# Optimization experiments

Hardware: AMD Instinct MI355X
Metric: run time of the kernel (lower is better)

The kernel has to match this reference:

```python
import jax, jax.numpy as jnp
import numpy as np

B, T, D, H = 2, 2048, 1024, 16
DK = D // H


def setup_inputs() -> dict:
    key = jax.random.key(0)
    ks = jax.random.split(key, 12)
    q = jax.random.normal(ks[0], (B, T, D), jnp.float32)
    k = jax.random.normal(ks[1], (B, T, D), jnp.float32)
    v = jax.random.normal(ks[2], (B, T, D), jnp.float32)
    # padding mask [B,1,T]: 1 = valid, 0 = pad (nonzero per torch eq(0) semantics)
    lengths = jnp.array([T, (3 * T) // 4])
    mask = (jnp.arange(T)[None, None, :] < lengths[:, None, None]).astype(jnp.int32)
    s = 0.02
    Wq = jax.random.normal(ks[3], (D, D), jnp.float32) * s
    Wk = jax.random.normal(ks[4], (D, D), jnp.float32) * s
    Wv = jax.random.normal(ks[5], (D, D), jnp.float32) * s
    Wo = jax.random.normal(ks[6], (D, D), jnp.float32) * s
    bq = jnp.zeros((D,), jnp.float32)
    bk = jnp.zeros((D,), jnp.float32)
    bv = jnp.zeros((D,), jnp.float32)
    bo = jnp.zeros((D,), jnp.float32)
    return {"query": q, "key": k, "value": v, "mask": mask,
            "Wq": Wq, "bq": bq, "Wk": Wk, "bk": bk,
            "Wv": Wv, "bv": bv, "Wo": Wo, "bo": bo}


def reference(query, key, value, mask, Wq, bq, Wk, bk, Wv, bv, Wo, bo):
    # q,k,v projections -> [B, H, T, DK]
    def proj(x, W, b):
        return (x @ W.T + b).reshape(B, T, H, DK).transpose(0, 2, 1, 3)
    q = proj(query, Wq, bq)
    k = proj(key, Wk, bk)
    v = proj(value, Wv, bv)
    scores = jnp.einsum("bhqd,bhkd->bhqk", q, k) * (DK ** -0.5)  # [B,H,T,T]
    m = (mask == 0)[:, None, :, :]  # [B,1,1,T] broadcast over heads/queries
    scores = jnp.where(m, -jnp.inf, scores)
    attn = jax.nn.softmax(scores, axis=-1)
    attn = jnp.where(m, 0.0, attn)
    x = jnp.einsum("bhqk,bhkd->bhqd", attn, v)  # [B,H,T,DK]
    x = x.transpose(0, 2, 1, 3).reshape(B, T, D)
    return x @ Wo.T + bo
```

## Files before the change

### kernel.cpp

```cpp
#include <hip/hip_runtime.h>

typedef unsigned short u16;
typedef unsigned int u32;
typedef __bf16 bf16x8 __attribute__((ext_vector_type(8)));
typedef float floatx4 __attribute__((ext_vector_type(4)));

#define BB 2
#define TT 2048
#define DD 1024
#define HH 16
#define DKK 64
#define ACT (BB * TT * DD)
#define WTE (DD * DD)

__device__ inline u16 f2bf(float f) {
    union { float f; u32 u; } c; c.f = f;
    u32 r = (c.u + 0x7fffu + ((c.u >> 16) & 1u)) >> 16;
    return (u16)r;
}
__device__ inline u32 pack2bf(float a, float b) {
    return (u32)f2bf(a) | ((u32)f2bf(b) << 16);
}

typedef __attribute__((address_space(1))) const u32 gas_u32;
typedef __attribute__((address_space(3))) u32 las_u32;
__device__ __forceinline__ void gl2lds16(const u16* g, u16* l) {
    __builtin_amdgcn_global_load_lds((gas_u32*)g, (las_u32*)l, 16, 0, 0);
}

struct CvtArgs { const float* src[7]; u16* dst[7]; };
__global__ __launch_bounds__(256) void convert_bf16(CvtArgs a) {
    int bid = blockIdx.x, t, local;
    if (bid < 768) { t = bid >> 8; local = bid & 255; }
    else { int r = bid - 768; t = 3 + (r >> 6); local = r & 63; }
    const float* s = a.src[t];
    u16* d = a.dst[t];
    const int base = local * 16384;
    for (int i = 0; i < 8; i++) {
        const int idx = base + i * 2048 + threadIdx.x * 8;
        float4 x0 = *(const float4*)(s + idx);
        float4 x1 = *(const float4*)(s + idx + 4);
        uint4 p;
        p.x = pack2bf(x0.x, x0.y); p.y = pack2bf(x0.z, x0.w);
        p.z = pack2bf(x1.x, x1.y); p.w = pack2bf(x1.z, x1.w);
        *(uint4*)(d + idx) = p;
    }
}

__global__ __launch_bounds__(256) void qkv_gemm(
    const u16* __restrict__ Qc, const u16* __restrict__ Kc,
    const u16* __restrict__ Vc,
    const u16* __restrict__ Wqc, const u16* __restrict__ Wkc,
    const u16* __restrict__ Wvc,
    const float* __restrict__ bq, const float* __restrict__ bk,
    const float* __restrict__ bv,
    u16* __restrict__ ws)
{
    __shared__ __align__(16) u16 As[128 * 32];
    __shared__ __align__(16) u16 Bs[128 * 32];
    const int z = blockIdx.z;
    const u16* A = (z == 0) ? Qc : (z == 1) ? Kc : Vc;
    const u16* W = (z == 0) ? Wqc : (z == 1) ? Wkc : Wvc;
    const float* bias = (z == 0) ? bq : (z == 1) ? bk : bv;
    u16* out = ws + (size_t)z * ACT / 4;
    out = ws + (size_t)z * (size_t)BB * HH * TT * DKK;

    const int tid  = threadIdx.x;
    const int wave = tid >> 6, lane = tid & 63;
    const int quad = lane >> 4, l16 = lane & 15;
    const int wm = wave & 1, wn = wave >> 1;
    const int m0 = blockIdx.y * 128, n0 = blockIdx.x * 128;
    const int K = DD;

    const int lrow = lane >> 2, lcol = (lane & 3) * 8;
    const u16* Ag0 = A + (size_t)(m0 + wave * 16 + lrow) * K + lcol;
    const u16* Ag1 = A + (size_t)(m0 + 64 + wave * 16 + lrow) * K + lcol;
    const u16* Wg0 = W + (size_t)(n0 + wave * 16 + lrow) * K + lcol;
    const u16* Wg1 = W + (size_t)(n0 + 64 + wave * 16 + lrow) * K + lcol;
    u16* AsD0 = &As[(wave * 16) * 32];
    u16* AsD1 = &As[(64 + wave * 16) * 32];
    u16* BsD0 = &Bs[(wave * 16) * 32];
    u16* BsD1 = &Bs[(64 + wave * 16) * 32];

    floatx4 acc[4][4];
    for (int i = 0; i < 4; i++)
        for (int j = 0; j < 4; j++)
            acc[i][j] = floatx4{0.f, 0.f, 0.f, 0.f};

    for (int k0 = 0; k0 < K; k0 += 32) {
        __syncthreads();
        gl2lds16(Ag0 + k0, AsD0);
        gl2lds16(Ag1 + k0, AsD1);
        gl2lds16(Wg0 + k0, BsD0);
        gl2lds16(Wg1 + k0, BsD1);
        __syncthreads();

        bf16x8 af[4], bfr[4];
        for (int mi = 0; mi < 4; mi++)
            af[mi] = *(const bf16x8*)&As[(wm * 64 + mi * 16 + l16) * 32 + quad * 8];
        for (int ni = 0; ni < 4; ni++)
            bfr[ni] = *(const bf16x8*)&Bs[(wn * 64 + ni * 16 + l16) * 32 + quad * 8];
        for (int mi = 0; mi < 4; mi++)
            for (int ni = 0; ni < 4; ni++)
                acc[mi][ni] = __builtin_amdgcn_mfma_f32_16x16x32_bf16(
                    af[mi], bfr[ni], acc[mi][ni], 0, 0, 0);
    }

    for (int ni = 0; ni < 4; ni++) {
        const int n = n0 + wn * 64 + ni * 16 + l16;
        const float bv2 = bias[n];
        for (int mi = 0; mi < 4; mi++) {
            for (int vv = 0; vv < 4; vv++) {
                const int m = m0 + wm * 64 + mi * 16 + quad * 4 + vv;
                const float val = acc[mi][ni][vv] + bv2;
                const int b = m >> 11, t = m & 2047, h = n >> 6, dk = n & 63;
                if (z == 2)
                    out[(((size_t)(b * HH + h)) * DKK + dk) * TT + t] = f2bf(val);
                else
                    out[(((size_t)(b * HH + h)) * TT + t) * DKK + dk] = f2bf(val);
            }
        }
    }
}

__global__ __launch_bounds__(256) void out_gemm(
    const u16* __restrict__ Av, const u16* __restrict__ Wv,
    const float* __restrict__ bias, float* __restrict__ outv)
{
    __shared__ __align__(16) u16 As[128 * 32];
    __shared__ __align__(16) u16 Bs[128 * 32];
    const int tid  = threadIdx.x;
    const int wave = tid >> 6, lane = tid & 63;
    const int quad = lane >> 4, l16 = lane & 15;
    const int wm = wave & 1, wn = wave >> 1;
    const int m0 = blockIdx.y * 128, n0 = blockIdx.x * 128;
    const int K = DD, N = DD;

    const int lrow = lane >> 2, lcol = (lane & 3) * 8;
    const u16* Ag0 = Av + (size_t)(m0 + wave * 16 + lrow) * K + lcol;
    const u16* Ag1 = Av + (size_t)(m0 + 64 + wave * 16 + lrow) * K + lcol;
    const u16* Wg0 = Wv + (size_t)(n0 + wave * 16 + lrow) * K + lcol;
    const u16* Wg1 = Wv + (size_t)(n0 + 64 + wave * 16 + lrow) * K + lcol;
    u16* AsD0 = &As[(wave * 16) * 32];
    u16* AsD1 = &As[(64 + wave * 16) * 32];
    u16* BsD0 = &Bs[(wave * 16) * 32];
    u16* BsD1 = &Bs[(64 + wave * 16) * 32];

    floatx4 acc[4][4];
    for (int i = 0; i < 4; i++)
        for (int j = 0; j < 4; j++)
            acc[i][j] = floatx4{0.f, 0.f, 0.f, 0.f};

    for (int k0 = 0; k0 < K; k0 += 32) {
        __syncthreads();
        gl2lds16(Ag0 + k0, AsD0);
        gl2lds16(Ag1 + k0, AsD1);
        gl2lds16(Wg0 + k0, BsD0);
        gl2lds16(Wg1 + k0, BsD1);
        __syncthreads();

        bf16x8 af[4], bfr[4];
        for (int mi = 0; mi < 4; mi++)
            af[mi] = *(const bf16x8*)&As[(wm * 64 + mi * 16 + l16) * 32 + quad * 8];
        for (int ni = 0; ni < 4; ni++)
            bfr[ni] = *(const bf16x8*)&Bs[(wn * 64 + ni * 16 + l16) * 32 + quad * 8];
        for (int mi = 0; mi < 4; mi++)
            for (int ni = 0; ni < 4; ni++)
                acc[mi][ni] = __builtin_amdgcn_mfma_f32_16x16x32_bf16(
                    af[mi], bfr[ni], acc[mi][ni], 0, 0, 0);
    }

    for (int ni = 0; ni < 4; ni++) {
        const int n = n0 + wn * 64 + ni * 16 + l16;
        const float bv2 = bias[n];
        for (int mi = 0; mi < 4; mi++)
            for (int vv = 0; vv < 4; vv++) {
                const int m = m0 + wm * 64 + mi * 16 + quad * 4 + vv;
                outv[(size_t)m * N + n] = acc[mi][ni][vv] + bv2;
            }
    }
}

__global__ __launch_bounds__(256) void attn_kernel(
    const u16* __restrict__ Qp, const u16* __restrict__ Kp,
    const u16* __restrict__ Vpt, const int* __restrict__ mask,
    u16* __restrict__ Xa)
{
    constexpr int LDK = 72, LDP = 72;
    __shared__ __align__(16) u16 Ks[64 * LDK];
    __shared__ __align__(16) u16 Vs[64 * LDK];
    __shared__ __align__(16) __bf16 Pl[4][32][LDP];
    const int tid  = threadIdx.x;
    const int wave = tid >> 6, lane = tid & 63;
    const int quad = lane >> 4, l16 = lane & 15;
    const int bid = blockIdx.x;
    const int qt = bid & 15, bh = bid >> 4;
    const int b = bh >> 4, h = bh & 15;
    const int qbase = qt * 128 + wave * 32;

    const u16* Qb = Qp + (size_t)bh * TT * DKK;
    const u16* Kb = Kp + (size_t)bh * TT * DKK;
    const u16* Vb = Vpt + (size_t)bh * DKK * TT;
    const int* mk = mask + b * TT;

    const int srow = tid >> 3, scol = (tid & 7) * 8;

    bf16x8 qf[2][2];
    for (int mb = 0; mb < 2; mb++) {
        qf[mb][0] = *(const bf16x8*)&Qb[(size_t)(qbase + mb * 16 + l16) * DKK + quad * 8];
        qf[mb][1] = *(const bf16x8*)&Qb[(size_t)(qbase + mb * 16 + l16) * DKK + 32 + quad * 8];
    }

    floatx4 o[2][4];
    float rsum[2][4];
    for (int mb = 0; mb < 2; mb++)
        for (int i = 0; i < 4; i++) {
            o[mb][i] = floatx4{0.f, 0.f, 0.f, 0.f};
            rsum[mb][i] = 0.f;
        }

    uint4 kr0 = *(const uint4*)&Kb[(size_t)srow * DKK + scol];
    uint4 kr1 = *(const uint4*)&Kb[(size_t)(32 + srow) * DKK + scol];
    uint4 vr0 = *(const uint4*)&Vb[(size_t)srow * TT + scol];
    uint4 vr1 = *(const uint4*)&Vb[(size_t)(32 + srow) * TT + scol];

    for (int ti = 0; ti < TT / 64; ti++) {
        const int k0 = ti * 64;
        __syncthreads();
        *(uint4*)&Ks[srow * LDK + scol] = kr0;
        *(uint4*)&Ks[(32 + srow) * LDK + scol] = kr1;
        *(uint4*)&Vs[srow * LDK + scol] = vr0;
        *(uint4*)&Vs[(32 + srow) * LDK + scol] = vr1;
        __syncthreads();
        if (ti + 1 < TT / 64) {
            kr0 = *(const uint4*)&Kb[(size_t)(k0 + 64 + srow) * DKK + scol];
            kr1 = *(const uint4*)&Kb[(size_t)(k0 + 96 + srow) * DKK + scol];
            vr0 = *(const uint4*)&Vb[(size_t)srow * TT + k0 + 64 + scol];
            vr1 = *(const uint4*)&Vb[(size_t)(32 + srow) * TT + k0 + 64 + scol];
        }

        const int mv0 = mk[k0 + l16];
        const int mv1 = mk[k0 + 16 + l16];
        const int mv2 = mk[k0 + 32 + l16];
        const int mv3 = mk[k0 + 48 + l16];
        if (!__any(mv0 | mv1 | mv2 | mv3)) continue;
        const float mf[4] = { mv0 ? 1.f : 0.f, mv1 ? 1.f : 0.f,
                              mv2 ? 1.f : 0.f, mv3 ? 1.f : 0.f };

        bf16x8 kf[4][2];
        for (int c = 0; c < 4; c++) {
            kf[c][0] = *(const bf16x8*)&Ks[(c * 16 + l16) * LDK + quad * 8];
            kf[c][1] = *(const bf16x8*)&Ks[(c * 16 + l16) * LDK + 32 + quad * 8];
        }

        for (int mb = 0; mb < 2; mb++) {
            floatx4 s[4];
            for (int c = 0; c < 4; c++) s[c] = floatx4{0.f, 0.f, 0.f, 0.f};
            for (int c = 0; c < 4; c++) {
                s[c] = __builtin_amdgcn_mfma_f32_16x16x32_bf16(qf[mb][0], kf[c][0], s[c], 0, 0, 0);
                s[c] = __builtin_amdgcn_mfma_f32_16x16x32_bf16(qf[mb][1], kf[c][1], s[c], 0, 0, 0);
            }
            for (int c = 0; c < 4; c++)
                for (int v = 0; v < 4; v++) {
                    const float p = __expf(s[c][v] * 0.125f) * mf[c];
                    rsum[mb][v] += p;
                    Pl[wave][mb * 16 + quad * 4 + v][c * 16 + l16] = (__bf16)p;
                }
        }
        __asm__ volatile("" ::: "memory");
        bf16x8 pf[2][2];
        for (int mb = 0; mb < 2; mb++) {
            pf[mb][0] = *(const bf16x8*)&Pl[wave][mb * 16 + l16][quad * 8];
            pf[mb][1] = *(const bf16x8*)&Pl[wave][mb * 16 + l16][32 + quad * 8];
        }
        __asm__ volatile("" ::: "memory");

        for (int nb = 0; nb < 4; nb++) {
            const bf16x8 vf0 = *(const bf16x8*)&Vs[(nb * 16 + l16) * LDK + quad * 8];
            const bf16x8 vf1 = *(const bf16x8*)&Vs[(nb * 16 + l16) * LDK + 32 + quad * 8];
            o[0][nb] = __builtin_amdgcn_mfma_f32_16x16x32_bf16(pf[0][0], vf0, o[0][nb], 0, 0, 0);
            o[0][nb] = __builtin_amdgcn_mfma_f32_16x16x32_bf16(pf[0][1], vf1, o[0][nb], 0, 0, 0);
            o[1][nb] = __builtin_amdgcn_mfma_f32_16x16x32_bf16(pf[1][0], vf0, o[1][nb], 0, 0, 0);
            o[1][nb] = __builtin_amdgcn_mfma_f32_16x16x32_bf16(pf[1][1], vf1, o[1][nb], 0, 0, 0);
        }
    }

    for (int off = 1; off < 16; off <<= 1)
        for (int mb = 0; mb < 2; mb++)
            for (int v = 0; v < 4; v++)
                rsum[mb][v] += __shfl_xor(rsum[mb][v], off, 64);

    for (int mb = 0; mb < 2; mb++) {
        float inv[4];
        for (int v = 0; v < 4; v++) inv[v] = 1.0f / rsum[mb][v];
        for (int nb = 0; nb < 4; nb++)
            for (int v = 0; v < 4; v++) {
                const int t = qbase + mb * 16 + quad * 4 + v;
                Xa[((size_t)b * TT + t) * DD + h * DKK + nb * 16 + l16] =
                    f2bf(o[mb][nb][v] * inv[v]);
            }
    }
}

extern "C" void kernel_launch(void* const* d_in, const int* in_sizes, int n_in,
                              void* d_out, int out_size, void* d_ws, size_t ws_size,
                              hipStream_t stream) {
    const float* q    = (const float*)d_in[0];
    const float* k    = (const float*)d_in[1];
    const float* v    = (const float*)d_in[2];
    const int*   mask = (const int*)d_in[3];
    const float* Wq   = (const float*)d_in[4];
    const float* bq   = (const float*)d_in[5];
    const float* Wk   = (const float*)d_in[6];
    const float* bk   = (const float*)d_in[7];
    const float* Wv   = (const float*)d_in[8];
    const float* bv   = (const float*)d_in[9];
    const float* Wo   = (const float*)d_in[10];
    const float* bo   = (const float*)d_in[11];

    u16* Qc  = (u16*)d_ws;
    u16* Kc  = Qc + (size_t)ACT;
    u16* Vc  = Kc + (size_t)ACT;
    u16* Wqc = Vc + (size_t)ACT;
    u16* Wkc = Wqc + (size_t)WTE;
    u16* Wvc = Wkc + (size_t)WTE;
    u16* Woc = Wvc + (size_t)WTE;
    u16* Qp  = Woc + (size_t)WTE;
    u16* Kp  = Qp + (size_t)ACT;
    u16* Vpt = Kp + (size_t)ACT;
    u16* Xa  = Vpt + (size_t)ACT;

    CvtArgs ca;
    ca.src[0] = q;  ca.dst[0] = Qc;
    ca.src[1] = k;  ca.dst[1] = Kc;
    ca.src[2] = v;  ca.dst[2] = Vc;
    ca.src[3] = Wq; ca.dst[3] = Wqc;
    ca.src[4] = Wk; ca.dst[4] = Wkc;
    ca.src[5] = Wv; ca.dst[5] = Wvc;
    ca.src[6] = Wo; ca.dst[6] = Woc;
    convert_bf16<<<1024, 256, 0, stream>>>(ca);

    qkv_gemm<<<dim3(DD / 128, (BB * TT) / 128, 3), 256, 0, stream>>>(
        Qc, Kc, Vc, Wqc, Wkc, Wvc, bq, bk, bv, Qp);

    attn_kernel<<<dim3(BB * HH * (TT / 128)), 256, 0, stream>>>(Qp, Kp, Vpt, mask, Xa);

    out_gemm<<<dim3(DD / 128, (BB * TT) / 128), 256, 0, stream>>>(Xa, Woc, bo, (float*)d_out);
}
```

Measured before the change: 251.9 us.

## Split attention query tile across eight waves with 16 rows each

The attention kernel now runs 512 threads per block, with each of eight waves handling 16 query rows instead of four waves handling 32. K/V tile loading is spread across twice as many threads, so each thread loads one row-chunk instead of two. This aims to raise wave-level parallelism and latency hiding per block and cut per-thread register pressure. In exchange, K/V fragments are reused across fewer query rows per wave, so LDS reads per MFMA roughly double. A dead duplicate pointer assignment in the QKV GEMM is also removed.

```diff
diff --git a/kernel.cpp b/kernel.cpp
--- a/kernel.cpp
+++ b/kernel.cpp
@@ -62,8 +62,7 @@
     const u16* A = (z == 0) ? Qc : (z == 1) ? Kc : Vc;
     const u16* W = (z == 0) ? Wqc : (z == 1) ? Wkc : Wvc;
     const float* bias = (z == 0) ? bq : (z == 1) ? bk : bv;
-    u16* out = ws + (size_t)z * ACT / 4;
-    out = ws + (size_t)z * (size_t)BB * HH * TT * DKK;
+    u16* out = ws + (size_t)z * (size_t)BB * HH * TT * DKK;
 
     const int tid  = threadIdx.x;
     const int wave = tid >> 6, lane = tid & 63;
@@ -181,7 +180,7 @@
     }
 }
 
-__global__ __launch_bounds__(256) void attn_kernel(
+__global__ __launch_bounds__(512) void attn_kernel(
     const u16* __restrict__ Qp, const u16* __restrict__ Kp,
     const u16* __restrict__ Vpt, const int* __restrict__ mask,
     u16* __restrict__ Xa)
@@ -189,14 +188,14 @@
     constexpr int LDK = 72, LDP = 72;
     __shared__ __align__(16) u16 Ks[64 * LDK];
     __shared__ __align__(16) u16 Vs[64 * LDK];
-    __shared__ __align__(16) __bf16 Pl[4][32][LDP];
+    __shared__ __align__(16) __bf16 Pl[8][16][LDP];
     const int tid  = threadIdx.x;
     const int wave = tid >> 6, lane = tid & 63;
     const int quad = lane >> 4, l16 = lane & 15;
     const int bid = blockIdx.x;
     const int qt = bid & 15, bh = bid >> 4;
     const int b = bh >> 4, h = bh & 15;
-    const int qbase = qt * 128 + wave * 32;
+    const int qbase = qt * 128 + wave * 16;
 
     const u16* Qb = Qp + (size_t)bh * TT * DKK;
     const u16* Kb = Kp + (size_t)bh * TT * DKK;
@@ -205,38 +204,28 @@
 
     const int srow = tid >> 3, scol = (tid & 7) * 8;
 
-    bf16x8 qf[2][2];
-    for (int mb = 0; mb < 2; mb++) {
-        qf[mb][0] = *(const bf16x8*)&Qb[(size_t)(qbase + mb * 16 + l16) * DKK + quad * 8];
-        qf[mb][1] = *(const bf16x8*)&Qb[(size_t)(qbase + mb * 16 + l16) * DKK + 32 + quad * 8];
-    }
-
-    floatx4 o[2][4];
-    float rsum[2][4];
-    for (int mb = 0; mb < 2; mb++)
-        for (int i = 0; i < 4; i++) {
-            o[mb][i] = floatx4{0.f, 0.f, 0.f, 0.f};
-            rsum[mb][i] = 0.f;
-        }
-
-    uint4 kr0 = *(const uint4*)&Kb[(size_t)srow * DKK + scol];
-    uint4 kr1 = *(const uint4*)&Kb[(size_t)(32 + srow) * DKK + scol];
-    uint4 vr0 = *(const uint4*)&Vb[(size_t)srow * TT + scol];
-    uint4 vr1 = *(const uint4*)&Vb[(size_t)(32 + srow) * TT + scol];
+    const bf16x8 qf0 = *(const bf16x8*)&Qb[(size_t)(qbase + l16) * DKK + quad * 8];
+    const bf16x8 qf1 = *(const bf16x8*)&Qb[(size_t)(qbase + l16) * DKK + 32 + quad * 8];
+
+    floatx4 o[4];
+    float rsum[4];
+    for (int i = 0; i < 4; i++) {
+        o[i] = floatx4{0.f, 0.f, 0.f, 0.f};
+        rsum[i] = 0.f;
+    }
+
+    uint4 kr = *(const uint4*)&Kb[(size_t)srow * DKK + scol];
+    uint4 vr = *(const uint4*)&Vb[(size_t)srow * TT + scol];
 
     for (int ti = 0; ti < TT / 64; ti++) {
         const int k0 = ti * 64;
         __syncthreads();
-        *(uint4*)&Ks[srow * LDK + scol] = kr0;
-        *(uint4*)&Ks[(32 + srow) * LDK + scol] = kr1;
-        *(uint4*)&Vs[srow * LDK + scol] = vr0;
-        *(uint4*)&Vs[(32 + srow) * LDK + scol] = vr1;
+        *(uint4*)&Ks[srow * LDK + scol] = kr;
+        *(uint4*)&Vs[srow * LDK + scol] = vr;
         __syncthreads();
         if (ti + 1 < TT / 64) {
-            kr0 = *(const uint4*)&Kb[(size_t)(k0 + 64 + srow) * DKK + scol];
-            kr1 = *(const uint4*)&Kb[(size_t)(k0 + 96 + srow) * DKK + scol];
-            vr0 = *(const uint4*)&Vb[(size_t)srow * TT + k0 + 64 + scol];
-            vr1 = *(const uint4*)&Vb[(size_t)(32 + srow) * TT + k0 + 64 + scol];
+            kr = *(const uint4*)&Kb[(size_t)(k0 + 64 + srow) * DKK + scol];
+            vr = *(const uint4*)&Vb[(size_t)srow * TT + k0 + 64 + scol];
         }
 
         const int mv0 = mk[k0 + l16];
@@ -253,53 +242,45 @@
             kf[c][1] = *(const bf16x8*)&Ks[(c * 16 + l16) * LDK + 32 + quad * 8];
         }
 
-        for (int mb = 0; mb < 2; mb++) {
-            floatx4 s[4];
-            for (int c = 0; c < 4; c++) s[c] = floatx4{0.f, 0.f, 0.f, 0.f};
-            for (int c = 0; c < 4; c++) {
-                s[c] = __builtin_amdgcn_mfma_f32_16x16x32_bf16(qf[mb][0], kf[c][0], s[c], 0, 0, 0);
-                s[c] = __builtin_amdgcn_mfma_f32_16x16x32_bf16(qf[mb][1], kf[c][1], s[c], 0, 0, 0);
+        floatx4 s[4];
+        for (int c = 0; c < 4; c++) s[c] = floatx4{0.f, 0.f, 0.f, 0.f};
+        for (int c = 0; c < 4; c++) {
+            s[c] = __builtin_amdgcn_mfma_f32_16x16x32_bf16(qf0, kf[c][0], s[c], 0, 0, 0);
+            s[c] = __builtin_amdgcn_mfma_f32_16x16x32_bf16(qf1, kf[c][1], s[c], 0, 0, 0);
+        }
+
+        for (int c = 0; c < 4; c++)
+            for (int v = 0; v < 4; v++) {
+                const float p = __expf(s[c][v] * 0.125f) * mf[c];
+                rsum[v] += p;
+                Pl[wave][quad * 4 + v][c * 16 + l16] = (__bf16)p;
             }
-            for (int c = 0; c < 4; c++)
-                for (int v = 0; v < 4; v++) {
-                    const float p = __expf(s[c][v] * 0.125f) * mf[c];
-                    rsum[mb][v] += p;
-                    Pl[wave][mb * 16 + quad * 4 + v][c * 16 + l16] = (__bf16)p;
-                }
-        }
+
         __asm__ volatile("" ::: "memory");
-        bf16x8 pf[2][2];
-        for (int mb = 0; mb < 2; mb++) {
-            pf[mb][0] = *(const bf16x8*)&Pl[wave][mb * 16 + l16][quad * 8];
-            pf[mb][1] = *(const bf16x8*)&Pl[wave][mb * 16 + l16][32 + quad * 8];
-        }
+        const bf16x8 pf0 = *(const bf16x8*)&Pl[wave][l16][quad * 8];
+        const bf16x8 pf1 = *(const bf16x8*)&Pl[wave][l16][32 + quad * 8];
         __asm__ volatile("" ::: "memory");
 
         for (int nb = 0; nb < 4; nb++) {
             const bf16x8 vf0 = *(const bf16x8*)&Vs[(nb * 16 + l16) * LDK + quad * 8];
             const bf16x8 vf1 = *(const bf16x8*)&Vs[(nb * 16 + l16) * LDK + 32 + quad * 8];
-            o[0][nb] = __builtin_amdgcn_mfma_f32_16x16x32_bf16(pf[0][0], vf0, o[0][nb], 0, 0, 0);
-            o[0][nb] = __builtin_amdgcn_mfma_f32_16x16x32_bf16(pf[0][1], vf1, o[0][nb], 0, 0, 0);
-            o[1][nb] = __builtin_amdgcn_mfma_f32_16x16x32_bf16(pf[1][0], vf0, o[1][nb], 0, 0, 0);
-            o[1][nb] = __builtin_amdgcn_mfma_f32_16x16x32_bf16(pf[1][1], vf1, o[1][nb], 0, 0, 0);
+            o[nb] = __builtin_amdgcn_mfma_f32_16x16x32_bf16(pf0, vf0, o[nb], 0, 0, 0);
+            o[nb] = __builtin_amdgcn_mfma_f32_16x16x32_bf16(pf1, vf1, o[nb], 0, 0, 0);
         }
     }
 
     for (int off = 1; off < 16; off <<= 1)
-        for (int mb = 0; mb < 2; mb++)
-            for (int v = 0; v < 4; v++)
-                rsum[mb][v] += __shfl_xor(rsum[mb][v], off, 64);
-
-    for (int mb = 0; mb < 2; mb++) {
-        float inv[4];
-        for (int v = 0; v < 4; v++) inv[v] = 1.0f / rsum[mb][v];
-        for (int nb = 0; nb < 4; nb++)
-            for (int v = 0; v < 4; v++) {
-                const int t = qbase + mb * 16 + quad * 4 + v;
-                Xa[((size_t)b * TT + t) * DD + h * DKK + nb * 16 + l16] =
-                    f2bf(o[mb][nb][v] * inv[v]);
-            }
-    }
+        for (int v = 0; v < 4; v++)
+            rsum[v] += __shfl_xor(rsum[v], off, 64);
+
+    float inv[4];
+    for (int v = 0; v < 4; v++) inv[v] = 1.0f / rsum[v];
+    for (int nb = 0; nb < 4; nb++)
+        for (int v = 0; v < 4; v++) {
+            const int t = qbase + quad * 4 + v;
+            Xa[((size_t)b * TT + t) * DD + h * DKK + nb * 16 + l16] =
+                f2bf(o[nb][v] * inv[v]);
+        }
 }
 
 extern "C" void kernel_launch(void* const* d_in, const int* in_sizes, int n_in,
@@ -343,7 +324,7 @@
     qkv_gemm<<<dim3(DD / 128, (BB * TT) / 128, 3), 256, 0, stream>>>(
         Qc, Kc, Vc, Wqc, Wkc, Wvc, bq, bk, bv, Qp);
 
-    attn_kernel<<<dim3(BB * HH * (TT / 128)), 256, 0, stream>>>(Qp, Kp, Vpt, mask, Xa);
+    attn_kernel<<<dim3(BB * HH * (TT / 128)), 512, 0, stream>>>(Qp, Kp, Vpt, mask, Xa);
 
     out_gemm<<<dim3(DD / 128, (BB * TT) / 128), 256, 0, stream>>>(Xa, Woc, bo, (float*)d_out);
 }
```

Measured after the change: 247.0 us. No clear change (-2.0%).
